# Kernel optimization log

Hardware: AMD Instinct MI355X
Metric: run time of the kernel (lower is better)

Reference implementation:

```python
import jax, jax.numpy as jnp
import numpy as np

N_NODES = 50000
D_FEAT = 512
H1, H2 = 128, 64
N_CLASSES = 40
E_MP = 800000
E_LP = 250000


def gcn_conv(x, W, b, edge_index, edge_weight, num_nodes):
    """PyG GCNConv: add self-loops, symmetric norm D^-1/2 (A+I) D^-1/2, then (norm-agg)(xW)+b."""
    row, col = edge_index[0], edge_index[1]
    loop = jnp.arange(num_nodes)
    row = jnp.concatenate([row, loop])
    col = jnp.concatenate([col, loop])
    ew = jnp.concatenate([edge_weight, jnp.ones((num_nodes,), x.dtype)])
    deg = jax.ops.segment_sum(ew, col, num_segments=num_nodes)
    dinv = jnp.where(deg > 0, deg ** -0.5, 0.0).astype(x.dtype)
    norm = dinv[row] * ew * dinv[col]  # [E+N]
    h = x @ W  # [N, out]
    msg = h[row] * norm[:, None]  # gather + scale per edge
    out = jax.ops.segment_sum(msg, col, num_segments=num_nodes) + b
    return out


def setup_inputs() -> dict:
    key = jax.random.key(0)
    ks = jax.random.split(key, 16)
    inp = {}
    inp["x"] = jax.random.normal(ks[0], (N_NODES, D_FEAT), jnp.float32)
    inp["train_pos_edge_index"] = jax.random.randint(ks[1], (2, E_MP), 0, N_NODES)
    inp["edge_index"] = jax.random.randint(ks[2], (2, E_MP), 0, N_NODES)
    inp["edge_weight"] = jax.random.uniform(ks[3], (E_MP,), jnp.float32)
    inp["pos_edge_index"] = jax.random.randint(ks[4], (2, E_LP), 0, N_NODES)
    inp["neg_edge_index"] = jax.random.randint(ks[5], (2, E_LP), 0, N_NODES)
    # parameters (glorot-ish scaled)
    def w(k, i, o):
        return jax.random.normal(k, (i, o), jnp.float32) * (2.0 / (i + o)) ** 0.5
    inp["W1"] = w(ks[6], D_FEAT, H1)
    inp["b1"] = jnp.zeros((H1,), jnp.float32)
    inp["W2"] = w(ks[7], H1, H2)
    inp["b2"] = jnp.zeros((H2,), jnp.float32)
    inp["W_attr"] = w(ks[8], H2, N_CLASSES)
    inp["b_attr"] = jnp.zeros((N_CLASSES,), jnp.float32)
    inp["W_att"] = w(ks[9], H2, N_CLASSES)
    inp["b_att"] = jnp.zeros((N_CLASSES,), jnp.float32)
    return inp


def reference(x, train_pos_edge_index, edge_index, edge_weight, pos_edge_index,
              neg_edge_index, W1, b1, W2, b2, W_attr, b_attr, W_att, b_att):
    ones = jnp.ones((train_pos_edge_index.shape[1],), x.dtype)
    h = jax.nn.relu(gcn_conv(x, W1, b1, train_pos_edge_index, ones, N_NODES))
    h = gcn_conv(h, W2, b2, train_pos_edge_index, ones, N_NODES)  # [N, 64]
    attr = gcn_conv(h, W_attr, b_attr, edge_index, edge_weight, N_NODES)
    # gradient reversal is identity in forward
    att = gcn_conv(h, W_att, b_att, edge_index, edge_weight, N_NODES)
    total = jnp.concatenate([pos_edge_index, neg_edge_index], axis=-1)  # [2, 2*E_LP]
    x_j = h[total[0]]
    x_i = h[total[1]]
    res = jnp.einsum("ef,ef->e", x_i, x_j)
    return res, jax.nn.log_softmax(attr, axis=1), jax.nn.log_softmax(att, axis=1)
```

## Files before the change

### kernel.cpp

```cpp
#include <hip/hip_runtime.h>

typedef short s16x8 __attribute__((ext_vector_type(8)));
typedef float f32x4 __attribute__((ext_vector_type(4)));

#define CPAD 16

static __device__ __forceinline__ unsigned short f2bf(float f) {
  unsigned u = __float_as_uint(f);
  u += 0x7fff + ((u >> 16) & 1);
  return (unsigned short)(u >> 16);
}
static __device__ __forceinline__ float bf2f(unsigned short h) {
  return __uint_as_float(((unsigned)h) << 16);
}


static __global__ void k_init(int* cntTp, int* cntEp, int n) {
  int i = blockIdx.x * blockDim.x + threadIdx.x;
  if (i < n) { cntTp[(size_t)i * CPAD] = 0; cntEp[(size_t)i * CPAD] = 0; }
}

static __global__ void k_count(const int* __restrict__ tcol, const int* __restrict__ ecol,
                               int* __restrict__ cntTp, int* __restrict__ cntEp,
                               int* __restrict__ rankT, int* __restrict__ rankE, int E) {
  int e = blockIdx.x * blockDim.x + threadIdx.x;
  if (e < E) {
    rankT[e] = atomicAdd(&cntTp[(size_t)tcol[e] * CPAD], 1);
    rankE[e] = atomicAdd(&cntEp[(size_t)ecol[e] * CPAD], 1);
  }
}

static __global__ void k_compact(const int* __restrict__ cntTp, const int* __restrict__ cntEp,
                                 int* __restrict__ cntT, int* __restrict__ cntE, int n) {
  int i = blockIdx.x * blockDim.x + threadIdx.x;
  if (i < n) { cntT[i] = cntTp[(size_t)i * CPAD]; cntE[i] = cntEp[(size_t)i * CPAD]; }
}

static __global__ __launch_bounds__(256) void k_scanA(
    const int* __restrict__ cntT, const int* __restrict__ cntE,
    int* __restrict__ bsum, int n, int nb) {
  const int* cnt = blockIdx.y ? cntE : cntT;
  int tid = threadIdx.x;
  int base = blockIdx.x * 1024 + tid * 4;
  int s = 0;
#pragma unroll
  for (int q = 0; q < 4; ++q) { int i = base + q; if (i < n) s += cnt[i]; }
  __shared__ int red[256];
  red[tid] = s;
  __syncthreads();
  for (int off = 128; off > 0; off >>= 1) {
    if (tid < off) red[tid] += red[tid + off];
    __syncthreads();
  }
  if (tid == 0) bsum[blockIdx.y * nb + blockIdx.x] = red[0];
}

static __global__ void k_scanB(int* bsum, int* ptrT, int* ptrE, int nb, int n) {
  int a = threadIdx.x;
  if (a > 1) return;
  int* bs = bsum + a * nb;
  int run = 0;
  for (int i = 0; i < nb; ++i) { int c = bs[i]; bs[i] = run; run += c; }
  (a ? ptrE : ptrT)[n] = run;
}

static __global__ __launch_bounds__(256) void k_scanC(
    const int* __restrict__ cntT, const int* __restrict__ cntE,
    const int* __restrict__ bsum, int* __restrict__ ptrT, int* __restrict__ ptrE,
    int n, int nb) {
  const int* cnt = blockIdx.y ? cntE : cntT;
  int* ptr = blockIdx.y ? ptrE : ptrT;
  int tid = threadIdx.x;
  int pre = bsum[blockIdx.y * nb + blockIdx.x];
  int base = blockIdx.x * 1024 + tid * 4;
  int v[4];
  int s = 0;
#pragma unroll
  for (int q = 0; q < 4; ++q) { int i = base + q; v[q] = (i < n) ? cnt[i] : 0; s += v[q]; }
  __shared__ int red[256];
  red[tid] = s;
  __syncthreads();
  for (int off = 1; off < 256; off <<= 1) {
    int t = (tid >= off) ? red[tid - off] : 0;
    __syncthreads();
    red[tid] += t;
    __syncthreads();
  }
  int run = pre + (tid ? red[tid - 1] : 0);
#pragma unroll
  for (int q = 0; q < 4; ++q) {
    int i = base + q;
    if (i < n) ptr[i] = run;
    run += v[q];
  }
}

static __global__ void k_dinvT(const int* __restrict__ cntT, float* __restrict__ dinvT, int n) {
  int i = blockIdx.x * blockDim.x + threadIdx.x;
  if (i < n) dinvT[i] = rsqrtf((float)cntT[i] + 1.0f);
}

static __global__ void k_fill(const int* __restrict__ trow, const int* __restrict__ tcol,
                              const int* __restrict__ erow, const int* __restrict__ ecol,
                              const float* __restrict__ ew, const float* __restrict__ dinvT,
                              const int* __restrict__ ptrT, const int* __restrict__ ptrE,
                              const int* __restrict__ rankT, const int* __restrict__ rankE,
                              int2* __restrict__ srcwT, int2* __restrict__ srcwE, int E) {
  int base = (blockIdx.x * blockDim.x + threadIdx.x) * 2;
  if (base + 1 < E) {
    int2 tr = *(const int2*)&trow[base];
    int2 tc = *(const int2*)&tcol[base];
    int2 er = *(const int2*)&erow[base];
    int2 ec = *(const int2*)&ecol[base];
    float2 w = *(const float2*)&ew[base];
    int2 rt = *(const int2*)&rankT[base];
    int2 re = *(const int2*)&rankE[base];
    int2 p;
    p.x = tr.x; p.y = __float_as_int(dinvT[tr.x]); srcwT[ptrT[tc.x] + rt.x] = p;
    p.x = tr.y; p.y = __float_as_int(dinvT[tr.y]); srcwT[ptrT[tc.y] + rt.y] = p;
    p.x = er.x; p.y = __float_as_int(w.x); srcwE[ptrE[ec.x] + re.x] = p;
    p.x = er.y; p.y = __float_as_int(w.y); srcwE[ptrE[ec.y] + re.y] = p;
  } else if (base < E) {
    int2 p;
    p.x = trow[base]; p.y = __float_as_int(dinvT[trow[base]]);
    srcwT[ptrT[tcol[base]] + rankT[base]] = p;
    p.x = erow[base]; p.y = __float_as_int(ew[base]);
    srcwE[ptrE[ecol[base]] + rankE[base]] = p;
  }
}

static __global__ void k_dinv2E(const int2* __restrict__ srcwE, const int* __restrict__ ptrE,
                                float* __restrict__ dinvE, int n) {
  int i = blockIdx.x * blockDim.x + threadIdx.x;
  if (i >= n) return;
  float s = 1.0f;
  int e = ptrE[i + 1];
  for (int j = ptrE[i]; j < e; ++j) s += __int_as_float(srcwE[j].y);
  dinvE[i] = rsqrtf(s);
}

static __global__ void k_wmulE(int2* __restrict__ srcwE, const float* __restrict__ dinvE, int E) {
  int base = (blockIdx.x * blockDim.x + threadIdx.x) * 2;
  if (base + 1 < E) {
    int4 q = *(const int4*)&srcwE[base];
    q.y = __float_as_int(__int_as_float(q.y) * dinvE[q.x]);
    q.w = __float_as_int(__int_as_float(q.w) * dinvE[q.z]);
    *(int4*)&srcwE[base] = q;
  } else if (base < E) {
    int2 p = srcwE[base];
    p.y = __float_as_int(__int_as_float(p.y) * dinvE[p.x]);
    srcwE[base] = p;
  }
}


static __global__ void k_cvtW(const float* __restrict__ W, unsigned short* __restrict__ Wh,
                              unsigned short* __restrict__ Wl, int K, int Nc) {
  int t = blockIdx.x * blockDim.x + threadIdx.x;
  if (t >= K * Nc) return;
  int k = t / Nc, c = t - k * Nc;
  float v = W[t];
  unsigned short hi = f2bf(v);
  size_t o = (size_t)(k >> 5) * (Nc * 32) + c * 32 + (k & 31);
  Wh[o] = hi;
  Wl[o] = f2bf(v - bf2f(hi));
}


#define GK 512
#define NKT 16

static __device__ __forceinline__ void cvt8(float4 a, float4 b, s16x8& hi, s16x8& lo) {
  float f[8] = {a.x, a.y, a.z, a.w, b.x, b.y, b.z, b.w};
#pragma unroll
  for (int i = 0; i < 8; ++i) {
    unsigned short h = f2bf(f[i]);
    hi[i] = (short)h;
    lo[i] = (short)f2bf(f[i] - bf2f(h));
  }
}

static __global__ __launch_bounds__(256, 2) void k_gemm_mfma_split(
    const float* __restrict__ A, const unsigned short* __restrict__ Bh,
    const unsigned short* __restrict__ Bl, float* __restrict__ C, int M) {
  int tid = threadIdx.x;
  int lane = tid & 63, wid = tid >> 6;
  int wr = wid >> 1, wc = wid & 1;
  int l15 = lane & 15, l4 = lane >> 4;
  int brow = blockIdx.x * 64;
  f32x4 acc[2][4] = {};

  const float* arow[2];
#pragma unroll
  for (int m = 0; m < 2; ++m) {
    int r = brow + wr * 32 + m * 16 + l15;
    arow[m] = &A[(size_t)min(r, M - 1) * GK + l4 * 8];
  }
  size_t boff = (size_t)(wc * 64 + l15) * 32 + l4 * 8;

#pragma unroll
  for (int kt = 0; kt < NKT; ++kt) {
    s16x8 afh[2], afl[2];
#pragma unroll
    for (int m = 0; m < 2; ++m) {
      float4 a0 = *(const float4*)(arow[m] + kt * 32);
      float4 a1 = *(const float4*)(arow[m] + kt * 32 + 4);
      cvt8(a0, a1, afh[m], afl[m]);
    }
    s16x8 bh[4], bl[4];
#pragma unroll
    for (int n = 0; n < 4; ++n) {
      size_t o = (size_t)kt * 4096 + boff + n * 512;
      bh[n] = *(const s16x8*)&Bh[o];
      bl[n] = *(const s16x8*)&Bl[o];
    }
#pragma unroll
    for (int m = 0; m < 2; ++m)
#pragma unroll
      for (int n = 0; n < 4; ++n) {
        acc[m][n] = __builtin_amdgcn_mfma_f32_16x16x32_bf16(afh[m], bh[n], acc[m][n], 0, 0, 0);
        acc[m][n] = __builtin_amdgcn_mfma_f32_16x16x32_bf16(afl[m], bh[n], acc[m][n], 0, 0, 0);
        acc[m][n] = __builtin_amdgcn_mfma_f32_16x16x32_bf16(afh[m], bl[n], acc[m][n], 0, 0, 0);
      }
  }

#pragma unroll
  for (int m = 0; m < 2; ++m) {
    int rbase = brow + wr * 32 + m * 16 + l4 * 4;
#pragma unroll
    for (int n = 0; n < 4; ++n) {
      int c = wc * 64 + n * 16 + l15;
#pragma unroll
      for (int j = 0; j < 4; ++j) {
        int r = rbase + j;
        if (r < M) C[(size_t)r * 128 + c] = acc[m][n][j];
      }
    }
  }
}


static __global__ __launch_bounds__(256, 2) void k_gemm_mfma64(
    const float* __restrict__ A, const unsigned short* __restrict__ Bh,
    const unsigned short* __restrict__ Bl, float* __restrict__ C, int M) {
  int tid = threadIdx.x;
  int lane = tid & 63, wid = tid >> 6;
  int wr = wid >> 1, wc = wid & 1;
  int l15 = lane & 15, l4 = lane >> 4;
  int brow = blockIdx.x * 64;
  f32x4 acc[2][2] = {};

  const float* arow[2];
#pragma unroll
  for (int m = 0; m < 2; ++m) {
    int r = brow + wr * 32 + m * 16 + l15;
    arow[m] = &A[(size_t)min(r, M - 1) * 128 + l4 * 8];
  }
  size_t boff = (size_t)(wc * 32 + l15) * 32 + l4 * 8;

#pragma unroll
  for (int kt = 0; kt < 4; ++kt) {
    s16x8 afh[2], afl[2];
#pragma unroll
    for (int m = 0; m < 2; ++m) {
      float4 a0 = *(const float4*)(arow[m] + kt * 32);
      float4 a1 = *(const float4*)(arow[m] + kt * 32 + 4);
      cvt8(a0, a1, afh[m], afl[m]);
    }
    s16x8 bh[2], bl[2];
#pragma unroll
    for (int n = 0; n < 2; ++n) {
      size_t o = (size_t)kt * 2048 + boff + n * 512;
      bh[n] = *(const s16x8*)&Bh[o];
      bl[n] = *(const s16x8*)&Bl[o];
    }
#pragma unroll
    for (int m = 0; m < 2; ++m)
#pragma unroll
      for (int n = 0; n < 2; ++n) {
        acc[m][n] = __builtin_amdgcn_mfma_f32_16x16x32_bf16(afh[m], bh[n], acc[m][n], 0, 0, 0);
        acc[m][n] = __builtin_amdgcn_mfma_f32_16x16x32_bf16(afl[m], bh[n], acc[m][n], 0, 0, 0);
        acc[m][n] = __builtin_amdgcn_mfma_f32_16x16x32_bf16(afh[m], bl[n], acc[m][n], 0, 0, 0);
      }
  }

#pragma unroll
  for (int m = 0; m < 2; ++m) {
    int rbase = brow + wr * 32 + m * 16 + l4 * 4;
#pragma unroll
    for (int n = 0; n < 2; ++n) {
      int c = wc * 32 + n * 16 + l15;
#pragma unroll
      for (int j = 0; j < 4; ++j) {
        int r = rbase + j;
        if (r < M) C[(size_t)r * 64 + c] = acc[m][n][j];
      }
    }
  }
}


template <int F, bool RELU>
static __global__ __launch_bounds__(256) void k_gather4(
    const float* __restrict__ H, const int* __restrict__ rowptr,
    const int2* __restrict__ srcw, const float* __restrict__ dinv,
    const float* __restrict__ Hpre, const float* __restrict__ bias,
    float* __restrict__ out, int n) {
  const int L = F / 4;
  int node = blockIdx.x * (256 / L) + threadIdx.x / L;
  if (node >= n) return;
  int f4 = (threadIdx.x % L) * 4;
  float d = dinv[node];
  float4 hp = *(const float4*)&Hpre[(size_t)node * F + f4];
  float ax = hp.x * d, ay = hp.y * d, az = hp.z * d, aw = hp.w * d;
  int j = rowptr[node], e = rowptr[node + 1];
  for (; j + 1 < e; j += 2) {
    int2 a = srcw[j], b = srcw[j + 1];
    float w0 = __int_as_float(a.y);
    float w1 = __int_as_float(b.y);
    float4 v0 = *(const float4*)&H[(size_t)a.x * F + f4];
    float4 v1 = *(const float4*)&H[(size_t)b.x * F + f4];
    ax += v0.x * w0 + v1.x * w1;
    ay += v0.y * w0 + v1.y * w1;
    az += v0.z * w0 + v1.z * w1;
    aw += v0.w * w0 + v1.w * w1;
  }
  if (j < e) {
    int2 a = srcw[j];
    float wj = __int_as_float(a.y);
    float4 v = *(const float4*)&H[(size_t)a.x * F + f4];
    ax += v.x * wj; ay += v.y * wj; az += v.z * wj; aw += v.w * wj;
  }
  float bx = 0, by = 0, bz = 0, bw = 0;
  if (bias) { float4 bb = *(const float4*)&bias[f4]; bx = bb.x; by = bb.y; bz = bb.z; bw = bb.w; }
  ax = ax * d + bx; ay = ay * d + by; az = az * d + bz; aw = aw * d + bw;
  if (RELU) { ax = fmaxf(ax, 0.f); ay = fmaxf(ay, 0.f); az = fmaxf(az, 0.f); aw = fmaxf(aw, 0.f); }
  float4 o; o.x = ax; o.y = ay; o.z = az; o.w = aw;
  *(float4*)&out[(size_t)node * F + f4] = o;
}


static __global__ __launch_bounds__(256) void k_heads(
    const float* __restrict__ H, const float* __restrict__ Wattr,
    const float* __restrict__ battr, const float* __restrict__ Watt,
    const float* __restrict__ batt, float* __restrict__ out_attr,
    float* __restrict__ out_att, int n) {
  __shared__ float Hs[64][65];
  __shared__ float Ws[64][80];
  __shared__ float bs[80];
  __shared__ float Os[64][82];
  int tid = threadIdx.x;
  int node0 = blockIdx.x * 64;
  for (int i = tid; i < 1024; i += 256) {
    int r = i >> 4, c4 = (i & 15) * 4;
    float4 v = (node0 + r < n) ? *(const float4*)&H[(size_t)(node0 + r) * 64 + c4]
                               : make_float4(0.f, 0.f, 0.f, 0.f);
    Hs[r][c4] = v.x; Hs[r][c4 + 1] = v.y; Hs[r][c4 + 2] = v.z; Hs[r][c4 + 3] = v.w;
  }
  for (int i = tid; i < 64 * 40; i += 256) {
    int k = i / 40, j = i - k * 40;
    Ws[k][j] = Wattr[i];
    Ws[k][40 + j] = Watt[i];
  }
  if (tid < 40) { bs[tid] = battr[tid]; bs[40 + tid] = batt[tid]; }
  __syncthreads();

  int r = tid & 63, g = tid >> 6;
  float acc[20];
#pragma unroll
  for (int j = 0; j < 20; ++j) acc[j] = bs[g * 20 + j];
  for (int k = 0; k < 64; ++k) {
    float h = Hs[r][k];
#pragma unroll
    for (int j = 0; j < 20; ++j) acc[j] += h * Ws[k][g * 20 + j];
  }
#pragma unroll
  for (int j = 0; j < 20; ++j) Os[r][g * 20 + j] = acc[j];
  __syncthreads();

  if (tid < 128 && node0 + (tid & 63) < n) {
    int r2 = tid & 63;
    int base = (tid >> 6) * 40;
    float m = -1e30f;
    for (int j = 0; j < 40; ++j) m = fmaxf(m, Os[r2][base + j]);
    float s = 0.f;
    for (int j = 0; j < 40; ++j) s += expf(Os[r2][base + j] - m);
    float ls = logf(s) + m;
    float* o = (tid < 64 ? out_attr : out_att) + (size_t)(node0 + r2) * 40;
    for (int j = 0; j < 40; ++j) o[j] = Os[r2][base + j] - ls;
  }
}


static __global__ __launch_bounds__(256) void k_linkpred4(
    const float* __restrict__ H2, const int* __restrict__ pos,
    const int* __restrict__ neg, float* __restrict__ res, int Elp) {
  int t = blockIdx.x * 256 + threadIdx.x;
  int e = t >> 4, f4 = (t & 15) * 4;
  if (e >= 2 * Elp) return;
  int a, b;
  if (e < Elp) { a = pos[e]; b = pos[Elp + e]; }
  else { int e2 = e - Elp; a = neg[e2]; b = neg[Elp + e2]; }
  float4 va = *(const float4*)&H2[(size_t)a * 64 + f4];
  float4 vb = *(const float4*)&H2[(size_t)b * 64 + f4];
  float p = va.x * vb.x + va.y * vb.y + va.z * vb.z + va.w * vb.w;
  p += __shfl_xor(p, 1);
  p += __shfl_xor(p, 2);
  p += __shfl_xor(p, 4);
  p += __shfl_xor(p, 8);
  if ((t & 15) == 0) res[e] = p;
}


extern "C" void kernel_launch(void* const* d_in, const int* in_sizes, int n_in,
                              void* d_out, int out_size, void* d_ws, size_t ws_size,
                              hipStream_t stream) {
  const float* x    = (const float*)d_in[0];
  const int*   tp   = (const int*)d_in[1];
  const int*   ei   = (const int*)d_in[2];
  const float* ew   = (const float*)d_in[3];
  const int*   pos  = (const int*)d_in[4];
  const int*   neg  = (const int*)d_in[5];
  const float* W1   = (const float*)d_in[6];
  const float* b1   = (const float*)d_in[7];
  const float* W2   = (const float*)d_in[8];
  const float* b2   = (const float*)d_in[9];
  const float* Wattr= (const float*)d_in[10];
  const float* battr= (const float*)d_in[11];
  const float* Watt = (const float*)d_in[12];
  const float* batt = (const float*)d_in[13];

  const int N   = in_sizes[0] / 512;
  const int EMP = in_sizes[1] / 2;
  const int ELP = in_sizes[4] / 2;
  const int NB  = (N + 1023) / 1024;

  float* ws = (float*)d_ws;
  float* dinvT = ws;
  float* dinvE = dinvT + N;
  int* rowptrT = (int*)(dinvE + N);
  int* rowptrE = rowptrT + (N + 4);
  int2* srcwT  = (int2*)(rowptrE + (N + 4));
  int2* srcwE  = srcwT + EMP;
  int* bsum    = (int*)(srcwE + EMP);
  unsigned short* W1h = (unsigned short*)(bsum + 128);
  unsigned short* W1l = W1h + 512 * 128;
  unsigned short* W2h = W1l + 512 * 128;
  unsigned short* W2l = W2h + 128 * 64;
  float* bufA  = (float*)(W2l + 128 * 64);
  float* bufB  = bufA + (size_t)N * 128;
  float* bufC  = bufB + (size_t)N * 128;
  int* rankT = (int*)bufA;
  int* rankE = rankT + EMP;
  int* cntTp = (int*)bufB;
  int* cntEp = cntTp + (size_t)N * CPAD;
  int* cntT  = cntEp + (size_t)N * CPAD;
  int* cntE  = cntT + N;

  float* out_res  = (float*)d_out;
  float* out_attr = out_res + 2 * (size_t)ELP;
  float* out_att  = out_attr + (size_t)N * 40;

  dim3 b256(256);
  int gN = (N + 255) / 256;
  int gE1 = (EMP + 255) / 256;
  int gE2 = (EMP + 511) / 512;

  k_init<<<gN, b256, 0, stream>>>(cntTp, cntEp, N);
  k_cvtW<<<(512 * 128 + 255) / 256, b256, 0, stream>>>(W1, W1h, W1l, 512, 128);
  k_cvtW<<<(128 * 64 + 255) / 256, b256, 0, stream>>>(W2, W2h, W2l, 128, 64);
  k_count<<<gE1, b256, 0, stream>>>(tp + EMP, ei + EMP, cntTp, cntEp, rankT, rankE, EMP);
  k_compact<<<gN, b256, 0, stream>>>(cntTp, cntEp, cntT, cntE, N);
  k_dinvT<<<gN, b256, 0, stream>>>(cntT, dinvT, N);
  {
    dim3 gs(NB, 2);
    k_scanA<<<gs, b256, 0, stream>>>(cntT, cntE, bsum, N, NB);
    k_scanB<<<1, 64, 0, stream>>>(bsum, rowptrT, rowptrE, NB, N);
    k_scanC<<<gs, b256, 0, stream>>>(cntT, cntE, bsum, rowptrT, rowptrE, N, NB);
  }
  k_fill<<<gE2, b256, 0, stream>>>(tp, tp + EMP, ei, ei + EMP, ew, dinvT,
                                   rowptrT, rowptrE, rankT, rankE, srcwT, srcwE, EMP);
  k_dinv2E<<<gN, b256, 0, stream>>>(srcwE, rowptrE, dinvE, N);
  k_wmulE<<<(EMP + 511) / 512, b256, 0, stream>>>(srcwE, dinvE, EMP);

  k_gemm_mfma_split<<<(N + 63) / 64, b256, 0, stream>>>(x, W1h, W1l, bufA, N);
  k_gather4<128, true><<<(N + 7) / 8, b256, 0, stream>>>(
      bufA, rowptrT, srcwT, dinvT, bufA, b1, bufB, N);

  k_gemm_mfma64<<<(N + 63) / 64, b256, 0, stream>>>(bufB, W2h, W2l, bufA, N);
  k_gather4<64, false><<<(N + 15) / 16, b256, 0, stream>>>(
      bufA, rowptrT, srcwT, dinvT, bufA, b2, bufC, N);

  k_gather4<64, false><<<(N + 15) / 16, b256, 0, stream>>>(
      bufC, rowptrE, srcwE, dinvE, bufC, nullptr, bufA, N);

  k_heads<<<(N + 63) / 64, b256, 0, stream>>>(
      bufA, Wattr, battr, Watt, batt, out_attr, out_att, N);

  k_linkpred4<<<(2 * ELP * 16 + 255) / 256, b256, 0, stream>>>(bufC, pos, neg, out_res, ELP);
}
```

Measured before the change: 431.6 us.

## Stage first-layer GEMM tiles through double-buffered LDS with async global-to-LDS loads

The first GCN layer GEMM now copies A (fp32) and the split bf16 W1 tiles into double-buffered shared memory using global_load_lds. The copy for the next K step is issued before the MFMAs of the current step, instead of each wave loading operands straight from global memory. W1 is written in a swizzled layout, and the A tile uses an XOR swizzle, to avoid LDS bank conflicts. The aim is to hide global load latency behind compute, at the cost of 48KB of LDS per block, which may limit occupancy, plus a barrier on every K step.

Result: faster. 403.7 us (-6.5%).

```diff
diff --git a/kernel.cpp b/kernel.cpp
--- a/kernel.cpp
+++ b/kernel.cpp
@@ -155,13 +155,19 @@
 
 
 static __global__ void k_cvtW(const float* __restrict__ W, unsigned short* __restrict__ Wh,
-                              unsigned short* __restrict__ Wl, int K, int Nc) {
+                              unsigned short* __restrict__ Wl, int K, int Nc, int swizzled) {
   int t = blockIdx.x * blockDim.x + threadIdx.x;
   if (t >= K * Nc) return;
   int k = t / Nc, c = t - k * Nc;
   float v = W[t];
   unsigned short hi = f2bf(v);
-  size_t o = (size_t)(k >> 5) * (Nc * 32) + c * 32 + (k & 31);
+  int kk = k & 31;
+  if (swizzled) {
+    int q = kk >> 3, j = kk & 7;
+    int sw = (c & 3) ^ ((c >> 2) & 3);
+    kk = ((q ^ sw) << 3) + j;
+  }
+  size_t o = (size_t)(k >> 5) * (Nc * 32) + (size_t)c * 32 + kk;
   Wh[o] = hi;
   Wl[o] = f2bf(v - bf2f(hi));
 }
@@ -183,6 +189,9 @@
 static __global__ __launch_bounds__(256, 2) void k_gemm_mfma_split(
     const float* __restrict__ A, const unsigned short* __restrict__ Bh,
     const unsigned short* __restrict__ Bl, float* __restrict__ C, int M) {
+  __shared__ __align__(16) float          AfS[2][2048];
+  __shared__ __align__(16) unsigned short BhS[2][4096];
+  __shared__ __align__(16) unsigned short BlS[2][4096];
   int tid = threadIdx.x;
   int lane = tid & 63, wid = tid >> 6;
   int wr = wid >> 1, wc = wid & 1;
@@ -190,30 +199,63 @@
   int brow = blockIdx.x * 64;
   f32x4 acc[2][4] = {};
 
-  const float* arow[2];
-#pragma unroll
-  for (int m = 0; m < 2; ++m) {
-    int r = brow + wr * 32 + m * 16 + l15;
-    arow[m] = &A[(size_t)min(r, M - 1) * GK + l4 * 8];
-  }
-  size_t boff = (size_t)(wc * 64 + l15) * 32 + l4 * 8;
+  int idx0 = wid * 2, idx1 = wid * 2 + 1;
+  int arow0 = idx0 * 8 + (lane >> 3);
+  int arow1 = idx1 * 8 + (lane >> 3);
+  int achk = ((lane & 7) ^ (lane >> 3)) << 2;
+  const float* asrc0 = &A[(size_t)min(brow + arow0, M - 1) * GK + achk];
+  const float* asrc1 = &A[(size_t)min(brow + arow1, M - 1) * GK + achk];
+  const unsigned short* bhsrc0 = &Bh[idx0 * 512 + lane * 8];
+  const unsigned short* bhsrc1 = &Bh[idx1 * 512 + lane * 8];
+  const unsigned short* blsrc0 = &Bl[idx0 * 512 + lane * 8];
+  const unsigned short* blsrc1 = &Bl[idx1 * 512 + lane * 8];
+
+#define STG(buf, kt)                                                                       \
+  do {                                                                                     \
+    __builtin_amdgcn_global_load_lds(                                                      \
+        (const __attribute__((address_space(1))) void*)(asrc0 + (kt) * 32),                \
+        (__attribute__((address_space(3))) void*)&AfS[buf][idx0 * 256], 16, 0, 0);         \
+    __builtin_amdgcn_global_load_lds(                                                      \
+        (const __attribute__((address_space(1))) void*)(asrc1 + (kt) * 32),                \
+        (__attribute__((address_space(3))) void*)&AfS[buf][idx1 * 256], 16, 0, 0);         \
+    __builtin_amdgcn_global_load_lds(                                                      \
+        (const __attribute__((address_space(1))) void*)(bhsrc0 + (size_t)(kt) * 4096),     \
+        (__attribute__((address_space(3))) void*)&BhS[buf][idx0 * 512], 16, 0, 0);         \
+    __builtin_amdgcn_global_load_lds(                                                      \
+        (const __attribute__((address_space(1))) void*)(bhsrc1 + (size_t)(kt) * 4096),     \
+        (__attribute__((address_space(3))) void*)&BhS[buf][idx1 * 512], 16, 0, 0);         \
+    __builtin_amdgcn_global_load_lds(                                                      \
+        (const __attribute__((address_space(1))) void*)(blsrc0 + (size_t)(kt) * 4096),     \
+        (__attribute__((address_space(3))) void*)&BlS[buf][idx0 * 512], 16, 0, 0);         \
+    __builtin_amdgcn_global_load_lds(                                                      \
+        (const __attribute__((address_space(1))) void*)(blsrc1 + (size_t)(kt) * 4096),     \
+        (__attribute__((address_space(3))) void*)&BlS[buf][idx1 * 512], 16, 0, 0);         \
+  } while (0)
+
+  STG(0, 0);
 
 #pragma unroll
   for (int kt = 0; kt < NKT; ++kt) {
+    const int S = kt & 1;
+    __syncthreads();
     s16x8 afh[2], afl[2];
 #pragma unroll
     for (int m = 0; m < 2; ++m) {
-      float4 a0 = *(const float4*)(arow[m] + kt * 32);
-      float4 a1 = *(const float4*)(arow[m] + kt * 32 + 4);
+      int row = wr * 32 + m * 16 + l15;
+      int swr = row & 7;
+      float4 a0 = *(const float4*)&AfS[S][row * 32 + (((2 * l4) ^ swr) << 2)];
+      float4 a1 = *(const float4*)&AfS[S][row * 32 + (((2 * l4 + 1) ^ swr) << 2)];
       cvt8(a0, a1, afh[m], afl[m]);
     }
     s16x8 bh[4], bl[4];
 #pragma unroll
     for (int n = 0; n < 4; ++n) {
-      size_t o = (size_t)kt * 4096 + boff + n * 512;
-      bh[n] = *(const s16x8*)&Bh[o];
-      bl[n] = *(const s16x8*)&Bl[o];
+      int c = wc * 64 + n * 16 + l15;
+      int q = l4 ^ ((c & 3) ^ ((c >> 2) & 3));
+      bh[n] = *(const s16x8*)&BhS[S][c * 32 + q * 8];
+      bl[n] = *(const s16x8*)&BlS[S][c * 32 + q * 8];
     }
+    if (kt + 1 < NKT) STG(S ^ 1, kt + 1);
 #pragma unroll
     for (int m = 0; m < 2; ++m)
 #pragma unroll
@@ -223,6 +265,7 @@
         acc[m][n] = __builtin_amdgcn_mfma_f32_16x16x32_bf16(afh[m], bl[n], acc[m][n], 0, 0, 0);
       }
   }
+#undef STG
 
 #pragma unroll
   for (int m = 0; m < 2; ++m) {
@@ -467,8 +510,8 @@
   int gE2 = (EMP + 511) / 512;
 
   k_init<<<gN, b256, 0, stream>>>(cntTp, cntEp, N);
-  k_cvtW<<<(512 * 128 + 255) / 256, b256, 0, stream>>>(W1, W1h, W1l, 512, 128);
-  k_cvtW<<<(128 * 64 + 255) / 256, b256, 0, stream>>>(W2, W2h, W2l, 128, 64);
+  k_cvtW<<<(512 * 128 + 255) / 256, b256, 0, stream>>>(W1, W1h, W1l, 512, 128, 1);
+  k_cvtW<<<(128 * 64 + 255) / 256, b256, 0, stream>>>(W2, W2h, W2l, 128, 64, 0);
   k_count<<<gE1, b256, 0, stream>>>(tp + EMP, ei + EMP, cntTp, cntEp, rankT, rankE, EMP);
   k_compact<<<gN, b256, 0, stream>>>(cntTp, cntEp, cntT, cntE, N);
   k_dinvT<<<gN, b256, 0, stream>>>(cntT, dinvT, N);
```

## Co-schedule edge counting with first GEMM and fuse aggregation with link prediction

Applied to the files above, without the earlier changes.

The atomic degree-count kernel now runs inside the first GEMM launch: one block in five does GEMM tiles and the other four do grid-strided atomic counting, so the latency-bound atomics overlap with MFMA work. The rank buffers move out of bufA into a separate workspace region so the GEMM output no longer collides with them. The last gather kernel and the link-prediction kernel are merged into one launch split by block index, which removes a launch and lets both memory-bound phases share the GPU. The costs are a larger workspace and a fixed 4:1 block ratio that may not balance the two kinds of work.

Result: faster. 403.0 us (-6.6%).

```diff
diff --git a/kernel.cpp b/kernel.cpp
--- a/kernel.cpp
+++ b/kernel.cpp
@@ -18,16 +18,6 @@
 static __global__ void k_init(int* cntTp, int* cntEp, int n) {
   int i = blockIdx.x * blockDim.x + threadIdx.x;
   if (i < n) { cntTp[(size_t)i * CPAD] = 0; cntEp[(size_t)i * CPAD] = 0; }
-}
-
-static __global__ void k_count(const int* __restrict__ tcol, const int* __restrict__ ecol,
-                               int* __restrict__ cntTp, int* __restrict__ cntEp,
-                               int* __restrict__ rankT, int* __restrict__ rankE, int E) {
-  int e = blockIdx.x * blockDim.x + threadIdx.x;
-  if (e < E) {
-    rankT[e] = atomicAdd(&cntTp[(size_t)tcol[e] * CPAD], 1);
-    rankE[e] = atomicAdd(&cntEp[(size_t)ecol[e] * CPAD], 1);
-  }
 }
 
 static __global__ void k_compact(const int* __restrict__ cntTp, const int* __restrict__ cntEp,
@@ -161,11 +151,10 @@
   int k = t / Nc, c = t - k * Nc;
   float v = W[t];
   unsigned short hi = f2bf(v);
-  size_t o = (size_t)(k >> 5) * (Nc * 32) + c * 32 + (k & 31);
+  size_t o = (size_t)(k >> 5) * (Nc * 32) + (size_t)c * 32 + (k & 31);
   Wh[o] = hi;
   Wl[o] = f2bf(v - bf2f(hi));
 }
-
 
 #define GK 512
 #define NKT 16
@@ -180,14 +169,28 @@
   }
 }
 
-static __global__ __launch_bounds__(256, 2) void k_gemm_mfma_split(
+
+static __global__ __launch_bounds__(256, 2) void k_gemm_count(
     const float* __restrict__ A, const unsigned short* __restrict__ Bh,
-    const unsigned short* __restrict__ Bl, float* __restrict__ C, int M) {
+    const unsigned short* __restrict__ Bl, float* __restrict__ C, int M, int NG,
+    const int* __restrict__ tcol, const int* __restrict__ ecol,
+    int* __restrict__ cntTp, int* __restrict__ cntEp,
+    int* __restrict__ rankT, int* __restrict__ rankE, int E) {
+  int bid = blockIdx.x;
+  if (bid % 5 != 0) {
+    int cb = bid - bid / 5 - 1;
+    int ncb = gridDim.x - NG;
+    for (int e = cb * 256 + threadIdx.x; e < E; e += ncb * 256) {
+      rankT[e] = atomicAdd(&cntTp[(size_t)tcol[e] * CPAD], 1);
+      rankE[e] = atomicAdd(&cntEp[(size_t)ecol[e] * CPAD], 1);
+    }
+    return;
+  }
   int tid = threadIdx.x;
   int lane = tid & 63, wid = tid >> 6;
   int wr = wid >> 1, wc = wid & 1;
   int l15 = lane & 15, l4 = lane >> 4;
-  int brow = blockIdx.x * 64;
+  int brow = (bid / 5) * 64;
   f32x4 acc[2][4] = {};
 
   const float* arow[2];
@@ -340,6 +343,59 @@
 }
 
 
+static __global__ __launch_bounds__(256) void k_gather_lp(
+    const float* __restrict__ H, const int* __restrict__ rowptr,
+    const int2* __restrict__ srcw, const float* __restrict__ dinv,
+    float* __restrict__ outAgg, int n, int NGa,
+    const int* __restrict__ pos, const int* __restrict__ neg,
+    float* __restrict__ res, int Elp) {
+  int bid = blockIdx.x;
+  if (bid < NGa) {
+    int node = bid * 16 + threadIdx.x / 16;
+    if (node >= n) return;
+    int f4 = (threadIdx.x % 16) * 4;
+    float d = dinv[node];
+    float4 hp = *(const float4*)&H[(size_t)node * 64 + f4];
+    float ax = hp.x * d, ay = hp.y * d, az = hp.z * d, aw = hp.w * d;
+    int j = rowptr[node], e = rowptr[node + 1];
+    for (; j + 1 < e; j += 2) {
+      int2 a = srcw[j], b = srcw[j + 1];
+      float w0 = __int_as_float(a.y);
+      float w1 = __int_as_float(b.y);
+      float4 v0 = *(const float4*)&H[(size_t)a.x * 64 + f4];
+      float4 v1 = *(const float4*)&H[(size_t)b.x * 64 + f4];
+      ax += v0.x * w0 + v1.x * w1;
+      ay += v0.y * w0 + v1.y * w1;
+      az += v0.z * w0 + v1.z * w1;
+      aw += v0.w * w0 + v1.w * w1;
+    }
+    if (j < e) {
+      int2 a = srcw[j];
+      float wj = __int_as_float(a.y);
+      float4 v = *(const float4*)&H[(size_t)a.x * 64 + f4];
+      ax += v.x * wj; ay += v.y * wj; az += v.z * wj; aw += v.w * wj;
+    }
+    float4 o; o.x = ax * d; o.y = ay * d; o.z = az * d; o.w = aw * d;
+    *(float4*)&outAgg[(size_t)node * 64 + f4] = o;
+  } else {
+    int t = (bid - NGa) * 256 + threadIdx.x;
+    int e = t >> 4, f4 = (t & 15) * 4;
+    if (e >= 2 * Elp) return;
+    int a, b;
+    if (e < Elp) { a = pos[e]; b = pos[Elp + e]; }
+    else { int e2 = e - Elp; a = neg[e2]; b = neg[Elp + e2]; }
+    float4 va = *(const float4*)&H[(size_t)a * 64 + f4];
+    float4 vb = *(const float4*)&H[(size_t)b * 64 + f4];
+    float p = va.x * vb.x + va.y * vb.y + va.z * vb.z + va.w * vb.w;
+    p += __shfl_xor(p, 1);
+    p += __shfl_xor(p, 2);
+    p += __shfl_xor(p, 4);
+    p += __shfl_xor(p, 8);
+    if ((t & 15) == 0) res[e] = p;
+  }
+}
+
+
 static __global__ __launch_bounds__(256) void k_heads(
     const float* __restrict__ H, const float* __restrict__ Wattr,
     const float* __restrict__ battr, const float* __restrict__ Watt,
@@ -389,26 +445,6 @@
     float* o = (tid < 64 ? out_attr : out_att) + (size_t)(node0 + r2) * 40;
     for (int j = 0; j < 40; ++j) o[j] = Os[r2][base + j] - ls;
   }
-}
-
-
-static __global__ __launch_bounds__(256) void k_linkpred4(
-    const float* __restrict__ H2, const int* __restrict__ pos,
-    const int* __restrict__ neg, float* __restrict__ res, int Elp) {
-  int t = blockIdx.x * 256 + threadIdx.x;
-  int e = t >> 4, f4 = (t & 15) * 4;
-  if (e >= 2 * Elp) return;
-  int a, b;
-  if (e < Elp) { a = pos[e]; b = pos[Elp + e]; }
-  else { int e2 = e - Elp; a = neg[e2]; b = neg[Elp + e2]; }
-  float4 va = *(const float4*)&H2[(size_t)a * 64 + f4];
-  float4 vb = *(const float4*)&H2[(size_t)b * 64 + f4];
-  float p = va.x * vb.x + va.y * vb.y + va.z * vb.z + va.w * vb.w;
-  p += __shfl_xor(p, 1);
-  p += __shfl_xor(p, 2);
-  p += __shfl_xor(p, 4);
-  p += __shfl_xor(p, 8);
-  if ((t & 15) == 0) res[e] = p;
 }
 
 
@@ -434,6 +470,8 @@
   const int EMP = in_sizes[1] / 2;
   const int ELP = in_sizes[4] / 2;
   const int NB  = (N + 1023) / 1024;
+  const int NG  = (N + 63) / 64;
+  const int NGa = (N + 15) / 16;
 
   float* ws = (float*)d_ws;
   float* dinvT = ws;
@@ -450,7 +488,7 @@
   float* bufA  = (float*)(W2l + 128 * 64);
   float* bufB  = bufA + (size_t)N * 128;
   float* bufC  = bufB + (size_t)N * 128;
-  int* rankT = (int*)bufA;
+  int* rankT = (int*)(bufC + (size_t)N * 64);
   int* rankE = rankT + EMP;
   int* cntTp = (int*)bufB;
   int* cntEp = cntTp + (size_t)N * CPAD;
@@ -463,13 +501,16 @@
 
   dim3 b256(256);
   int gN = (N + 255) / 256;
-  int gE1 = (EMP + 255) / 256;
   int gE2 = (EMP + 511) / 512;
 
   k_init<<<gN, b256, 0, stream>>>(cntTp, cntEp, N);
   k_cvtW<<<(512 * 128 + 255) / 256, b256, 0, stream>>>(W1, W1h, W1l, 512, 128);
   k_cvtW<<<(128 * 64 + 255) / 256, b256, 0, stream>>>(W2, W2h, W2l, 128, 64);
-  k_count<<<gE1, b256, 0, stream>>>(tp + EMP, ei + EMP, cntTp, cntEp, rankT, rankE, EMP);
+
+  k_gemm_count<<<NG * 5, b256, 0, stream>>>(x, W1h, W1l, bufA, N, NG,
+                                            tp + EMP, ei + EMP, cntTp, cntEp,
+                                            rankT, rankE, EMP);
+
   k_compact<<<gN, b256, 0, stream>>>(cntTp, cntEp, cntT, cntE, N);
   k_dinvT<<<gN, b256, 0, stream>>>(cntT, dinvT, N);
   {
@@ -483,7 +524,6 @@
   k_dinv2E<<<gN, b256, 0, stream>>>(srcwE, rowptrE, dinvE, N);
   k_wmulE<<<(EMP + 511) / 512, b256, 0, stream>>>(srcwE, dinvE, EMP);
 
-  k_gemm_mfma_split<<<(N + 63) / 64, b256, 0, stream>>>(x, W1h, W1l, bufA, N);
   k_gather4<128, true><<<(N + 7) / 8, b256, 0, stream>>>(
       bufA, rowptrT, srcwT, dinvT, bufA, b1, bufB, N);
 
@@ -491,11 +531,9 @@
   k_gather4<64, false><<<(N + 15) / 16, b256, 0, stream>>>(
       bufA, rowptrT, srcwT, dinvT, bufA, b2, bufC, N);
 
-  k_gather4<64, false><<<(N + 15) / 16, b256, 0, stream>>>(
-      bufC, rowptrE, srcwE, dinvE, bufC, nullptr, bufA, N);
+  k_gather_lp<<<NGa + (2 * ELP * 16 + 255) / 256, b256, 0, stream>>>(
+      bufC, rowptrE, srcwE, dinvE, bufA, N, NGa, pos, neg, out_res, ELP);
 
   k_heads<<<(N + 63) / 64, b256, 0, stream>>>(
       bufA, Wattr, battr, Watt, batt, out_attr, out_att, N);
-
-  k_linkpred4<<<(2 * ELP * 16 + 255) / 256, b256, 0, stream>>>(bufC, pos, neg, out_res, ELP);
-}
+}
```
